# Kernel optimization log

Hardware: AMD Instinct MI355X
Metric: run time of the kernel (lower is better)

The kernel has to match this reference:

```python
import jax, jax.numpy as jnp
import numpy as np

B, Q, C, P, A = 32, 300, 81, 300, 29


def box_cxcywh_to_xyxy(b):
    cx, cy, w, h = b[..., 0], b[..., 1], b[..., 2], b[..., 3]
    return jnp.stack([cx - 0.5 * w, cy - 0.5 * h, cx + 0.5 * w, cy + 0.5 * h], axis=-1)


def setup_inputs() -> dict:
    key = jax.random.key(0)
    k1, k2, k3, k4, k5 = jax.random.split(key, 5)
    pred_logits = jax.random.normal(k1, (B, Q, C), dtype=jnp.float32)
    pred_boxes = jax.random.uniform(k2, (B, Q, 4), dtype=jnp.float32)
    pred_actions = jax.random.normal(k3, (B, P, A), dtype=jnp.float32)
    pred_rel_pairs = jax.random.randint(k4, (B, P, 2), 0, Q, dtype=jnp.int64)
    # realistic image sizes (h, w) in pixels
    target_sizes = 480.0 + 320.0 * jax.random.uniform(k5, (B, 2), dtype=jnp.float32)
    return {
        'pred_logits': pred_logits,
        'pred_boxes': pred_boxes,
        'pred_actions': pred_actions,
        'pred_rel_pairs': pred_rel_pairs,
        'target_sizes': target_sizes,
    }


def reference(pred_logits, pred_boxes, pred_actions, pred_rel_pairs, target_sizes):
    threshold = 0.0
    # class scores/labels (last class is no-object, excluded from max)
    prob = jax.nn.softmax(pred_logits, axis=-1)
    scores = prob[..., :-1].max(-1)          # [B,Q]
    labels = prob[..., :-1].argmax(-1)       # [B,Q]
    # boxes to xyxy, scaled to image size
    boxes = box_cxcywh_to_xyxy(pred_boxes)   # [B,Q,4]
    img_h, img_w = target_sizes[:, 0], target_sizes[:, 1]
    scale_fct = jnp.stack([img_w, img_h, img_w, img_h], axis=1)  # [B,4]
    boxes = boxes * scale_fct[:, None, :]
    # vcoco path: pairwise action score matrix via one fused scatter
    pair_actions = jax.nn.sigmoid(pred_actions)          # [B,P,A]
    h_idx = pred_rel_pairs[:, :, 0]                      # [B,P]
    o_idx = pred_rel_pairs[:, :, 1]                      # [B,P]
    # original: if h_idx == o_idx -> o_idx = -1 (i.e. last column K of K+1)
    o_idx = jnp.where(h_idx == o_idx, Q, o_idx)
    b_idx = jnp.arange(B, dtype=h_idx.dtype)[:, None]    # [B,1] -> broadcast [B,P]
    score = jnp.zeros((B, Q, Q + 1, A), dtype=pair_actions.dtype)
    score = score.at[b_idx, h_idx, o_idx].set(pair_actions)
    score = jnp.transpose(score, (0, 3, 1, 2))           # [B,A,Q,Q+1]
    # ragged boolean masks (returned as masks instead of data-dependent slices)
    h_mask = (labels == 1) & (scores > threshold)        # human rows
    o_mask = jnp.concatenate([scores > threshold,
                              jnp.ones((B, 1), dtype=bool)], axis=1)  # K+1 cols
    return scores, labels, boxes, score, h_mask, o_mask
```

## Files before the change

kernel.cpp:

```cpp
#include <hip/hip_runtime.h>
#include <hip/hip_bf16.h>

#define BB 32
#define QQ 300
#define CC 81
#define PP 300
#define AA 29

constexpr long long OFF_SCORES = 0;
constexpr long long OFF_LABELS = OFF_SCORES + (long long)BB * QQ;
constexpr long long OFF_BOXES  = OFF_LABELS + (long long)BB * QQ;
constexpr long long OFF_SCORE  = OFF_BOXES  + (long long)BB * QQ * 4;
constexpr long long SCORE_ELEMS = (long long)BB * AA * QQ * (QQ + 1);
constexpr long long OFF_HMASK  = OFF_SCORE + SCORE_ELEMS;
constexpr long long OFF_OMASK  = OFF_HMASK + (long long)BB * QQ;

__global__ void cls_box_mask_kernel(const float* __restrict__ logits,
                                    const float* __restrict__ boxes_in,
                                    const float* __restrict__ tsize,
                                    float* __restrict__ out) {
    int t = blockIdx.x * blockDim.x + threadIdx.x;
    if (t >= BB * QQ) return;
    int b = t / QQ;
    int q = t - b * QQ;

    const float* l = logits + (long long)t * CC;

    float m = -1e30f;
    float best = -1e30f;
    int am = 0;
    for (int c = 0; c < CC; ++c) {
        float x = l[c];
        m = fmaxf(m, x);
        if (c < CC - 1 && x > best) { best = x; am = c; }
    }
    float s = 0.0f;
    for (int c = 0; c < CC; ++c) {
        s += __expf(l[c] - m);
    }
    float score = __expf(best - m) / s;

    out[OFF_SCORES + t] = score;
    out[OFF_LABELS + t] = (float)am;

    float cx = boxes_in[4 * (long long)t + 0];
    float cy = boxes_in[4 * (long long)t + 1];
    float w  = boxes_in[4 * (long long)t + 2];
    float h  = boxes_in[4 * (long long)t + 3];
    float img_h = tsize[2 * b + 0];
    float img_w = tsize[2 * b + 1];
    out[OFF_BOXES + 4 * (long long)t + 0] = (cx - 0.5f * w) * img_w;
    out[OFF_BOXES + 4 * (long long)t + 1] = (cy - 0.5f * h) * img_h;
    out[OFF_BOXES + 4 * (long long)t + 2] = (cx + 0.5f * w) * img_w;
    out[OFF_BOXES + 4 * (long long)t + 3] = (cy + 0.5f * h) * img_h;

    out[OFF_HMASK + t] = (am == 1 && score > 0.0f) ? 1.0f : 0.0f;
    out[OFF_OMASK + (long long)b * (QQ + 1) + q] = (score > 0.0f) ? 1.0f : 0.0f;
    if (q == 0) out[OFF_OMASK + (long long)b * (QQ + 1) + QQ] = 1.0f;
}

__global__ void scatter_kernel(const int* __restrict__ pairs,
                               const float* __restrict__ actions,
                               float* __restrict__ out) {
    __shared__ int keys[PP];
    __shared__ int nz;
    int tid = threadIdx.x;
    if (tid == 0) nz = 0;
    __syncthreads();

    int local = 0;
    for (int i = tid; i < BB * PP; i += blockDim.x) local |= pairs[2 * i + 1];
    if (local) atomicOr(&nz, 1);
    __syncthreads();
    bool is64 = (nz == 0);

    int b = blockIdx.x;
    int p = tid;
    int h = -1, o = -1;
    if (p < PP) {
        if (is64) {
            h = pairs[((long long)(b * PP + p)) * 4 + 0];
            o = pairs[((long long)(b * PP + p)) * 4 + 2];
        } else {
            h = pairs[((long long)(b * PP + p)) * 2 + 0];
            o = pairs[((long long)(b * PP + p)) * 2 + 1];
        }
        if (h == o) o = QQ;
        keys[p] = h * (QQ + 1) + o;
    }
    __syncthreads();
    if (p >= PP) return;

    int k = keys[p];
    for (int p2 = p + 1; p2 < PP; ++p2) {
        if (keys[p2] == k) return;
    }

    const float* act = actions + (long long)(b * PP + p) * AA;
    long long base = OFF_SCORE + (long long)b * AA * QQ * (QQ + 1)
                   + (long long)h * (QQ + 1) + o;
    for (int a = 0; a < AA; ++a) {
        float x = act[a];
        float sg = 1.0f / (1.0f + __expf(-x));
        out[base + (long long)a * QQ * (QQ + 1)] = sg;
    }
}

extern "C" void kernel_launch(void* const* d_in, const int* in_sizes, int n_in,
                              void* d_out, int out_size, void* d_ws, size_t ws_size,
                              hipStream_t stream) {
    const float* logits   = (const float*)d_in[0];
    const float* boxes_in = (const float*)d_in[1];
    const float* actions  = (const float*)d_in[2];
    const int*   pairs    = (const int*)d_in[3];
    const float* tsize    = (const float*)d_in[4];
    float* out = (float*)d_out;

    hipMemsetAsync((char*)d_out + OFF_SCORE * sizeof(float), 0,
                   (size_t)SCORE_ELEMS * sizeof(float), stream);

    int n = BB * QQ;
    cls_box_mask_kernel<<<(n + 255) / 256, 256, 0, stream>>>(logits, boxes_in, tsize, out);
    scatter_kernel<<<BB, 320, 0, stream>>>(pairs, actions, out);
}
```

Before: 396.7 us.

## Replace memset+scatter with LUT-driven dense write of score tensor

Builds a per-batch lookup table in workspace that maps each (h,o) slot to its last writing pair, using atomicMax to reproduce last-write-wins semantics. A new dense kernel then writes every element of the large score tensor exactly once, emitting either zero or the sigmoid of the mapped action with 16-byte vector stores. This removes the separate full-tensor memset and the serial per-thread dedup loop of the old scatter kernel. In exchange it adds a lookup-table read per output plane and a dependency on enough workspace, with the old path kept as a fallback.

```diff
diff --git a/kernel.cpp b/kernel.cpp
--- a/kernel.cpp
+++ b/kernel.cpp
@@ -14,6 +14,44 @@
 constexpr long long SCORE_ELEMS = (long long)BB * AA * QQ * (QQ + 1);
 constexpr long long OFF_HMASK  = OFF_SCORE + SCORE_ELEMS;
 constexpr long long OFF_OMASK  = OFF_HMASK + (long long)BB * QQ;
+
+constexpr int SLOTS = QQ * (QQ + 1);
+constexpr int SLOT4 = SLOTS / 4;
+constexpr size_t LUT_BYTES = (size_t)BB * SLOTS * sizeof(int);
+
+typedef float f32x4 __attribute__((ext_vector_type(4)));
+
+__global__ __launch_bounds__(512) void lut_build_kernel(const int* __restrict__ pairs,
+                                                        int* __restrict__ lut) {
+    __shared__ int nz;
+    int tid = threadIdx.x;
+    int b = blockIdx.x;
+    if (tid == 0) nz = 0;
+    __syncthreads();
+
+    int local = 0;
+    for (int i = tid; i < BB * PP; i += blockDim.x) local |= pairs[2 * i + 1];
+    if (local) atomicOr(&nz, 1);
+
+    int4* lb4 = (int4*)(lut + b * SLOTS);
+    int4 m1 = make_int4(-1, -1, -1, -1);
+    for (int i = tid; i < SLOT4; i += blockDim.x) lb4[i] = m1;
+    __syncthreads();
+    bool is64 = (nz == 0);
+
+    if (tid < PP) {
+        int h, o;
+        if (is64) {
+            h = pairs[((long long)(b * PP + tid)) * 4 + 0];
+            o = pairs[((long long)(b * PP + tid)) * 4 + 2];
+        } else {
+            h = pairs[((long long)(b * PP + tid)) * 2 + 0];
+            o = pairs[((long long)(b * PP + tid)) * 2 + 1];
+        }
+        if (h == o) o = QQ;
+        atomicMax(&lut[b * SLOTS + h * (QQ + 1) + o], tid);
+    }
+}
 
 __global__ void cls_box_mask_kernel(const float* __restrict__ logits,
                                     const float* __restrict__ boxes_in,
@@ -57,6 +95,30 @@
     out[OFF_HMASK + t] = (am == 1 && score > 0.0f) ? 1.0f : 0.0f;
     out[OFF_OMASK + (long long)b * (QQ + 1) + q] = (score > 0.0f) ? 1.0f : 0.0f;
     if (q == 0) out[OFF_OMASK + (long long)b * (QQ + 1) + QQ] = 1.0f;
+}
+
+__global__ __launch_bounds__(256) void score_write_kernel(const int* __restrict__ lut,
+                                                          const float* __restrict__ actions,
+                                                          float* __restrict__ out) {
+    int a = blockIdx.x;
+    int chunk = blockIdx.y;
+    int b = blockIdx.z;
+    const int4* lb4 = (const int4*)(lut + b * SLOTS);
+    const float* actb = actions + (long long)b * PP * AA + a;
+    f32x4* plane4 = (f32x4*)(out + OFF_SCORE + (long long)(b * AA + a) * SLOTS);
+
+    int s4 = chunk * 1024 + threadIdx.x;
+    #pragma unroll
+    for (int k = 0; k < 4; ++k, s4 += 256) {
+        if (s4 >= SLOT4) break;
+        int4 pi = lb4[s4];
+        f32x4 v = (f32x4)0.0f;
+        if (pi.x >= 0) v.x = 1.0f / (1.0f + __expf(-actb[pi.x * AA]));
+        if (pi.y >= 0) v.y = 1.0f / (1.0f + __expf(-actb[pi.y * AA]));
+        if (pi.z >= 0) v.z = 1.0f / (1.0f + __expf(-actb[pi.z * AA]));
+        if (pi.w >= 0) v.w = 1.0f / (1.0f + __expf(-actb[pi.w * AA]));
+        plane4[s4] = v;
+    }
 }
 
 __global__ void scatter_kernel(const int* __restrict__ pairs,
@@ -116,10 +178,16 @@
     const float* tsize    = (const float*)d_in[4];
     float* out = (float*)d_out;
 
-    hipMemsetAsync((char*)d_out + OFF_SCORE * sizeof(float), 0,
-                   (size_t)SCORE_ELEMS * sizeof(float), stream);
-
     int n = BB * QQ;
-    cls_box_mask_kernel<<<(n + 255) / 256, 256, 0, stream>>>(logits, boxes_in, tsize, out);
-    scatter_kernel<<<BB, 320, 0, stream>>>(pairs, actions, out);
+    if (d_ws != nullptr && ws_size >= LUT_BYTES) {
+        int* lut = (int*)d_ws;
+        lut_build_kernel<<<BB, 512, 0, stream>>>(pairs, lut);
+        cls_box_mask_kernel<<<(n + 255) / 256, 256, 0, stream>>>(logits, boxes_in, tsize, out);
+        score_write_kernel<<<dim3(AA, (SLOT4 + 1023) / 1024, BB), 256, 0, stream>>>(lut, actions, out);
+    } else {
+        hipMemsetAsync((char*)d_out + OFF_SCORE * sizeof(float), 0,
+                       (size_t)SCORE_ELEMS * sizeof(float), stream);
+        cls_box_mask_kernel<<<(n + 255) / 256, 256, 0, stream>>>(logits, boxes_in, tsize, out);
+        scatter_kernel<<<BB, 320, 0, stream>>>(pairs, actions, out);
+    }
 }
```

Measured after the change: 414.1 us. 1.04x slower.
